# Optimization experiments

Hardware: AMD Instinct MI355X
Metric: run time of the kernel (lower is better)

The kernel has to match this reference:

```python
import jax, jax.numpy as jnp
import numpy as np
from jax import lax

NUM_SEGMENTS = 50
HIDDEN = 128
IN_CH = 64
LOGSIG_DIM = IN_CH + IN_CH * (IN_CH - 1) // 2 + IN_CH  # level1 + Levy area + startpoint


def setup_inputs() -> dict:
    key = jax.random.key(0)
    k0, k1, k2, k3, k4 = jax.random.split(key, 5)
    B, C, T, V = 16, IN_CH, 200, 25
    x = jax.random.normal(k0, (B, C, T, V), dtype=jnp.float32)
    s = 1.0 / np.sqrt(HIDDEN).astype(np.float32)
    W_ih = jax.random.uniform(k1, (4 * HIDDEN, LOGSIG_DIM), jnp.float32, -s, s)
    W_hh = jax.random.uniform(k2, (4 * HIDDEN, HIDDEN), jnp.float32, -s, s)
    b_ih = jax.random.uniform(k3, (4 * HIDDEN,), jnp.float32, -s, s)
    b_hh = jax.random.uniform(k4, (4 * HIDDEN,), jnp.float32, -s, s)
    return {"x": x, "W_ih": W_ih, "W_hh": W_hh, "b_ih": b_ih, "b_hh": b_hh}


def _segment_logsig(xn):
    # xn: (N, C, T). Split T into NUM_SEGMENTS chunks; level-2 log-signature per chunk.
    N, C, T = xn.shape
    L = T // NUM_SEGMENTS  # points per segment
    p = xn.transpose(0, 2, 1).reshape(N, NUM_SEGMENTS, L, C)  # path points
    start = p[:, :, 0]                                  # (N,S,C) segment startpoint
    inc = p[:, :, 1:] - p[:, :, :-1]                    # (N,S,L-1,C) increments
    dev = p[:, :, :-1] - start[:, :, None]              # (N,S,L-1,C) p_t - p_0
    # Level-2 iterated integrals (cross terms): S2_ij = sum_t dev_t,i * inc_t,j
    S2 = jnp.einsum('nsti,nstj->nsij', dev, inc)        # (N,S,C,C)
    A = 0.5 * (S2 - S2.transpose(0, 1, 3, 2))           # Levy area (antisymmetric part)
    iu, ju = jnp.triu_indices(C, k=1)
    levy = A[:, :, iu, ju]                              # (N,S,C(C-1)/2)
    lvl1 = p[:, :, -1] - start                          # (N,S,C) level-1 term
    return jnp.concatenate([lvl1, levy, start], axis=-1)  # (N,S,LOGSIG_DIM)


def _lstm(seq, W_ih, W_hh, b_ih, b_hh):
    # seq: (N, S, F). Single-layer unidirectional LSTM, torch gate order (i,f,g,o).
    N = seq.shape[0]
    x_proj = jnp.einsum('nsf,gf->nsg', seq, W_ih) + b_ih + b_hh  # (N,S,4H)

    def step(carry, xt):
        h, c = carry
        gates = xt + h @ W_hh.T
        i, f, g, o = jnp.split(gates, 4, axis=-1)
        c = jax.nn.sigmoid(f) * c + jax.nn.sigmoid(i) * jnp.tanh(g)
        h = jax.nn.sigmoid(o) * jnp.tanh(c)
        return (h, c), h

    h0 = jnp.zeros((N, HIDDEN), seq.dtype)
    c0 = jnp.zeros((N, HIDDEN), seq.dtype)
    _, hs = lax.scan(step, (h0, c0), x_proj.transpose(1, 0, 2))
    return hs.transpose(1, 0, 2)  # (N,S,H)


def reference(x, W_ih, W_hh, b_ih, b_hh):
    B, C, T, V = x.shape
    xn = x.transpose(0, 3, 1, 2).reshape(B * V, C, T)
    ls = _segment_logsig(xn)                      # (B*V, S, LOGSIG_DIM)
    h = _lstm(ls, W_ih, W_hh, b_ih, b_hh)          # (B*V, S, H)
    out = h.reshape(B, V, NUM_SEGMENTS, HIDDEN).transpose(0, 3, 2, 1)
    return out  # (B, H, S, V)
```

## Files before the change

kernel.cpp:

```cpp
#include <hip/hip_runtime.h>
#include <stdint.h>

#define NSEG 50
#define HID 128
#define KDIM 2144
#define KD2 2240
#define KD2B 4480
#define NROW 20000
#define NROW_PAD 20096
#define GATES 512
#define NSEQ 400
#define NGRP 528

typedef __attribute__((ext_vector_type(8))) _Float16 f16x8;
typedef __attribute__((ext_vector_type(4))) _Float16 f16x4;
typedef __attribute__((ext_vector_type(4))) float f32x4;
typedef __attribute__((ext_vector_type(4))) uint32_t u32x4;

#define GLB_SPACE __attribute__((address_space(1)))
#define LDS_SPACE __attribute__((address_space(3)))

__device__ __forceinline__ void g2lds16(const void* g, void* l) {
    __builtin_amdgcn_global_load_lds((const GLB_SPACE uint32_t*)g,
                                     (LDS_SPACE uint32_t*)l, 16, 0, 0);
}

__device__ __forceinline__ int goff528(int i) {
    int n = 63 - i;
    int q = n >> 2, t = n & 3;
    return NGRP - (q + 1) * (2 * q + t);
}
__device__ __forceinline__ int ifromg(int g) {
    int i = 63 - (int)sqrtf(8.0f * (float)(NGRP - g));
    if (i < 0) i = 0;
    if (i > 62) i = 62;
    while (i > 0 && goff528(i) > g) i--;
    while (goff528(i + 1) <= g) i++;
    return i;
}

#define UVP(c) ((((c) & 3) << 4) | ((c) >> 2))

__global__ __launch_bounds__(512) void feat_kernel(const float* __restrict__ x,
                                                   const float* __restrict__ Wih,
                                                   const float* __restrict__ Whh,
                                                   const float* __restrict__ bih,
                                                   const float* __restrict__ bhh,
                                                   _Float16* __restrict__ feat,
                                                   _Float16* __restrict__ wh,
                                                   _Float16* __restrict__ whh16,
                                                   float* __restrict__ bias) {
    int bid = blockIdx.x;
    int tid = threadIdx.x;

    __shared__ float pbuf[64 * 101];
    __shared__ __align__(16) float4 uv4[25 * 64];

    if (bid >= 800) {
        int* kmap = (int*)pbuf;
        for (int k = tid; k < KD2; k += 512) {
            int orig;
            if (k < 64) {
                orig = k;
            } else if (k < 64 + 4 * NGRP) {
                int g = (k - 64) >> 2, p = (k - 64) & 3;
                int i = ifromg(g);
                int j = i + 1 + 4 * (g - goff528(i)) + p;
                orig = (j < 64) ? (64 + 63 * i - (i * (i - 1)) / 2 + (j - i - 1)) : -1;
            } else {
                orig = 2080 + (k - (64 + 4 * NGRP));
            }
            kmap[k] = orig;
        }
        __syncthreads();
        const int nwih = 512 * KD2;
        const int nwhh = 512 * HID;
        const int total = nwih + nwhh + 512;
        for (int idx = (bid - 800) * 512 + tid; idx < total; idx += 64 * 512) {
            if (idx < nwih) {
                int row = idx / KD2;
                int k = idx - row * KD2;
                int orig = kmap[k];
                wh[idx] = (orig >= 0) ? (_Float16)Wih[row * KDIM + orig] : (_Float16)0.0f;
            } else if (idx < nwih + nwhh) {
                int q = idx - nwih;
                whh16[q] = (_Float16)Whh[q];
            } else {
                int g = idx - nwih - nwhh;
                bias[g] = bih[g] + bhh[g];
            }
        }
        return;
    }

    int b = bid / NSEG;
    int s = bid - b * NSEG;

    for (int i = tid; i < 6400; i += 512) {
        int c = i / 100;
        int r = i - c * 100;
        pbuf[c * 101 + r] = x[(((size_t)b * 64 + c) * 200 + 4 * s) * 25 + r];
    }
    __syncthreads();

    for (int i = tid; i < 1600; i += 512) {
        int v = i >> 6;
        int c = i & 63;
        float p0 = pbuf[c * 101 + v];
        float p1 = pbuf[c * 101 + 25 + v];
        float p2 = pbuf[c * 101 + 50 + v];
        float p3 = pbuf[c * 101 + 75 + v];
        uv4[v * 64 + UVP(c)] = make_float4(p1 - p0, p2 - p0, p2 - p1, p3 - p2);
        size_t m = ((size_t)(b * 25 + v)) * NSEG + s;
        feat[m * KD2 + c] = (_Float16)(p3 - p0);
        feat[m * KD2 + (64 + 4 * NGRP) + c] = (_Float16)p0;
    }
    __syncthreads();

    for (int g = tid; g < NGRP; g += 512) {
        int i = ifromg(g);
        int t = g - goff528(i);
        int j0 = i + 1 + 4 * t;
        int k0 = 64 + 4 * g;
        float msk[4];
        int jc[4];
#pragma unroll
        for (int p = 0; p < 4; p++) {
            int j = j0 + p;
            msk[p] = (j < 64) ? 0.5f : 0.0f;
            jc[p] = (j < 64) ? UVP(j) : UVP(63);
        }
        int ip = UVP(i);
        for (int v = 0; v < 25; v++) {
            const float4* rowv = &uv4[v * 64];
            float4 a = rowv[ip];
            f16x4 o;
#pragma unroll
            for (int p = 0; p < 4; p++) {
                float4 bb = rowv[jc[p]];
                float val = msk[p] * (a.x * bb.z - bb.x * a.z + a.y * bb.w - bb.y * a.w);
                o[p] = (_Float16)val;
            }
            size_t m = ((size_t)(b * 25 + v)) * NSEG + s;
            *(f16x4*)(feat + m * KD2 + k0) = o;
        }
    }
}

__global__ __launch_bounds__(256, 4) void gemm_kernel(const _Float16* __restrict__ feat,
                                                      const _Float16* __restrict__ wh,
                                                      const float* __restrict__ bias,
                                                      _Float16* __restrict__ xproj2) {
    int bid = blockIdx.x;
    int x = bid & 7;
    int t = bid >> 3;
    int nb = t & 3;
    int mt = (t >> 2) * 8 + x;
    if (mt >= 157) return;
    int m0 = mt * 128;
    int n0 = nb * 128;
    int tid = threadIdx.x;
    int wave = tid >> 6;
    int lane = tid & 63;
    int quad = lane >> 4;
    int l15 = lane & 15;
    int wm = (wave >> 1) * 64;
    int wn = (wave & 1) * 64;

    int r8 = lane >> 3;
    int gcol = ((lane & 7) * 16) ^ (r8 * 16);

    __shared__ __align__(16) _Float16 smem[16896];
    char* As = (char*)smem;
    char* Bs = (char*)smem + 128 * 128;

    const f32x4 z4 = {0.f, 0.f, 0.f, 0.f};
    f32x4 acc[4][4];
    for (int i = 0; i < 4; i++)
        for (int j = 0; j < 4; j++) acc[i][j] = z4;

    const char* featB = (const char*)feat;
    const char* whB = (const char*)wh;

    for (int kt = 0; kt < 35; kt++) {
        size_t kb = (size_t)kt * 128;
        __syncthreads();
        for (int it = 0; it < 4; it++) {
            int rb = it * 32 + wave * 8;
            g2lds16(featB + (size_t)(m0 + rb + r8) * KD2B + kb + gcol, As + rb * 128);
            g2lds16(whB + (size_t)(n0 + rb + r8) * KD2B + kb + gcol, Bs + rb * 128);
        }
        __syncthreads();

        for (int ks = 0; ks < 2; ks++) {
            int off = ((ks * 64) | (quad * 16)) ^ ((l15 & 7) * 16);
            f16x8 af[4], bf[4];
            for (int tt = 0; tt < 4; tt++)
                af[tt] = *(const f16x8*)(As + (wm + tt * 16 + l15) * 128 + off);
            for (int tt = 0; tt < 4; tt++)
                bf[tt] = *(const f16x8*)(Bs + (wn + tt * 16 + l15) * 128 + off);
            for (int mtl = 0; mtl < 4; mtl++)
                for (int ntl = 0; ntl < 4; ntl++)
                    acc[mtl][ntl] = __builtin_amdgcn_mfma_f32_16x16x32_f16(af[mtl], bf[ntl], acc[mtl][ntl], 0, 0, 0);
        }
    }

    __syncthreads();
    for (int ntl = 0; ntl < 4; ntl++) {
        int nl = wn + ntl * 16 + l15;
        float bv = bias[n0 + nl];
        for (int mtl = 0; mtl < 4; mtl++)
            for (int r = 0; r < 4; r++) {
                int ml = wm + mtl * 16 + quad * 4 + r;
                smem[ml * 132 + nl] = (_Float16)(acc[mtl][ntl][r] + bv);
            }
    }
    __syncthreads();
    {
        int row = tid >> 1;
        int half = tid & 1;
        int m = m0 + row;
        if (m < NROW) {
            unsigned q = (unsigned)m / 50u;
            unsigned s = (unsigned)m - q * 50u;
            const char* src = (const char*)smem + row * 264 + half * 128;
            char* dst = (char*)xproj2 + ((size_t)s * NSEQ + q) * 1024 + (size_t)n0 * 2 + half * 128;
            for (int i = 0; i < 8; i++)
                *(u32x4*)(dst + i * 16) = *(const u32x4*)(src + i * 16);
        }
    }
}

__global__ __launch_bounds__(512, 2) void lstm_kernel(const _Float16* __restrict__ xproj2,
                                                      const _Float16* __restrict__ whh,
                                                      _Float16* __restrict__ hseq) {
    int bid = blockIdx.x;
    int tid = threadIdx.x;
    int wave = tid >> 6;
    int lane = tid & 63;
    int quad = lane >> 4;
    int col = lane & 15;
    int hid = wave * 16 + col;

    __shared__ __align__(16) char xbuf[25 * 4 * 1040];
    __shared__ __align__(16) _Float16 hst[NSEG * 4 * HID];
    __shared__ __align__(16) _Float16 hbuf[2][4 * 144];

    f16x8 bfrag[4][4];
    for (int g = 0; g < 4; g++) {
        int n = g * 128 + hid;
        for (int kq = 0; kq < 4; kq++)
            bfrag[g][kq] = *(const f16x8*)(whh + (size_t)n * HID + kq * 32 + quad * 8);
    }
    for (int i = tid; i < 2 * 4 * 144; i += 512) ((_Float16*)hbuf)[i] = (_Float16)0.0f;
    float cst = 0.0f;

    const char* xsrc = (const char*)xproj2;
    for (int r = wave; r < 100; r += 8)
        g2lds16(xsrc + ((size_t)((r >> 2) * NSEQ + bid * 4 + (r & 3))) * 1024 + lane * 16,
                xbuf + r * 1040);
    __syncthreads();

    const f32x4 z4 = {0.f, 0.f, 0.f, 0.f};
    for (int half = 0; half < 2; half++) {
        for (int ss = 0; ss < 25; ss++) {
            int s = half * 25 + ss;
            int cur = s & 1;
            int nxt = cur ^ 1;

            f16x8 afrag[4];
            for (int kq = 0; kq < 4; kq++)
                afrag[kq] = *(const f16x8*)(&hbuf[cur][(col & 3) * 144 + kq * 32 + quad * 8]);

            float xp[4];
            for (int g = 0; g < 4; g++)
                xp[g] = (float)(*(const _Float16*)(xbuf + (ss * 4 + quad) * 1040 +
                               (g * 128 + hid) * 2));

            f32x4 acc[4];
            for (int g = 0; g < 4; g++) {
                acc[g] = z4;
                for (int kq = 0; kq < 4; kq++)
                    acc[g] = __builtin_amdgcn_mfma_f32_16x16x32_f16(afrag[kq], bfrag[g][kq], acc[g], 0, 0, 0);
            }

            float gv[4];
            for (int g = 0; g < 4; g++) {
                float lo = (quad & 1) ? acc[g][1] : acc[g][0];
                float hi = (quad & 1) ? acc[g][3] : acc[g][2];
                gv[g] = (quad & 2) ? hi : lo;
            }

            float ip = gv[0] + xp[0];
            float fp = gv[1] + xp[1];
            float gp = gv[2] + xp[2];
            float op = gv[3] + xp[3];
            float si = __fdividef(1.0f, 1.0f + __expf(-ip));
            float sf = __fdividef(1.0f, 1.0f + __expf(-fp));
            float so = __fdividef(1.0f, 1.0f + __expf(-op));
            float eg = __expf(-2.0f * gp);
            float tg = __fdividef(1.0f - eg, 1.0f + eg);
            cst = sf * cst + si * tg;
            float ec = __expf(-2.0f * cst);
            float tc = __fdividef(1.0f - ec, 1.0f + ec);
            float hv = so * tc;
            _Float16 hv16 = (_Float16)hv;
            hbuf[nxt][quad * 144 + hid] = hv16;
            hst[(s * 4 + quad) * 128 + hid] = hv16;
            __syncthreads();
        }
        if (half == 0) {
            for (int r = wave; r < 100; r += 8)
                g2lds16(xsrc + ((size_t)((25 + (r >> 2)) * NSEQ + bid * 4 + (r & 3))) * 1024 + lane * 16,
                        xbuf + r * 1040);
            __syncthreads();
        }
    }

    const u32x4* src = (const u32x4*)hst;
    for (int i = tid; i < 3200; i += 512) {
        int s = i >> 6;
        int rem = i & 63;
        int seq = rem >> 4;
        int seg = rem & 15;
        u32x4 v = src[i];
        *(u32x4*)((char*)hseq + ((size_t)(s * NSEQ + bid * 4 + seq)) * 256 + seg * 16) = v;
    }
}

__global__ __launch_bounds__(256) void tr_kernel(const _Float16* __restrict__ hseq,
                                                 float* __restrict__ out) {
    int bid = blockIdx.x;
    int b = bid / NSEG;
    int s = bid - b * NSEG;
    int tid = threadIdx.x;

    __shared__ _Float16 buf[25 * 130];

    const uint32_t* src32 = (const uint32_t*)(hseq + ((size_t)s * NSEQ + b * 25) * HID);
    uint32_t* buf32 = (uint32_t*)buf;
    for (int i = tid; i < 1600; i += 256) {
        int v = i >> 6;
        int d = i & 63;
        buf32[v * 65 + d] = src32[i];
    }
    __syncthreads();
    for (int i = tid; i < 3200; i += 256) {
        int hid = i / 25;
        int v = i - hid * 25;
        out[(((size_t)b * 128 + hid) * NSEG + s) * 25 + v] = (float)buf[v * 130 + hid];
    }
}

extern "C" void kernel_launch(void* const* d_in, const int* in_sizes, int n_in,
                              void* d_out, int out_size, void* d_ws, size_t ws_size,
                              hipStream_t stream) {
    const float* x = (const float*)d_in[0];
    const float* Wih = (const float*)d_in[1];
    const float* Whh = (const float*)d_in[2];
    const float* bih = (const float*)d_in[3];
    const float* bhh = (const float*)d_in[4];
    float* out = (float*)d_out;

    char* ws = (char*)d_ws;
    size_t off = 0;
    _Float16* feat = (_Float16*)(ws + off);   off += (size_t)NROW_PAD * KD2 * 2;
    _Float16* xproj2 = (_Float16*)(ws + off); off += (size_t)NSEG * NSEQ * GATES * 2;
    _Float16* hseq = (_Float16*)(ws + off);   off += (size_t)NSEG * NSEQ * HID * 2;
    _Float16* wh = (_Float16*)(ws + off);     off += (size_t)512 * KD2 * 2;
    _Float16* whh16 = (_Float16*)(ws + off);  off += (size_t)512 * HID * 2;
    float* bias = (float*)(ws + off);         off += 512 * 4;

    hipLaunchKernelGGL(feat_kernel, dim3(864), dim3(512), 0, stream,
                       x, Wih, Whh, bih, bhh, feat, wh, whh16, bias);
    hipLaunchKernelGGL(gemm_kernel, dim3(640), dim3(256), 0, stream, feat, wh, bias, xproj2);
    hipLaunchKernelGGL(lstm_kernel, dim3(100), dim3(512), 0, stream, xproj2, whh16, hseq);
    hipLaunchKernelGGL(tr_kernel, dim3(16 * NSEG), dim3(256), 0, stream, hseq, out);
}
```

Baseline: 212.7 us.

## Double-buffer GEMM LDS tiles and split logsig Levy work across v-blocks

The GEMM kernel now uses two LDS buffers so the async global-to-LDS load of the next K tile is issued before computing on the current one, which cuts one barrier per iteration and overlaps load with MFMA. Launch bounds drop to 2 blocks per CU to fit the doubled shared memory. The logsig kernel's Levy-area loop is split over four groups of v values so more threads in each block do useful work. The trade-off is lower occupancy in the GEMM.

```diff
diff --git a/kernel.cpp b/kernel.cpp
--- a/kernel.cpp
+++ b/kernel.cpp
@@ -117,7 +117,9 @@
     }
     __syncthreads();
 
-    for (int g = tid; g < NGRP; g += 512) {
+    for (int idx = tid; idx < 4 * NGRP; idx += 512) {
+        int vb = idx / NGRP;
+        int g = idx - vb * NGRP;
         int i = ifromg(g);
         int t = g - goff528(i);
         int j0 = i + 1 + 4 * t;
@@ -131,7 +133,10 @@
             jc[p] = (j < 64) ? UVP(j) : UVP(63);
         }
         int ip = UVP(i);
-        for (int v = 0; v < 25; v++) {
+        int v0 = (vb == 0) ? 0 : 6 * vb + 1;
+        int vn = (vb == 0) ? 7 : 6;
+        for (int vv = 0; vv < vn; vv++) {
+            int v = v0 + vv;
             const float4* rowv = &uv4[v * 64];
             float4 a = rowv[ip];
             f16x4 o;
@@ -147,7 +152,7 @@
     }
 }
 
-__global__ __launch_bounds__(256, 4) void gemm_kernel(const _Float16* __restrict__ feat,
+__global__ __launch_bounds__(256, 2) void gemm_kernel(const _Float16* __restrict__ feat,
                                                       const _Float16* __restrict__ wh,
                                                       const float* __restrict__ bias,
                                                       _Float16* __restrict__ xproj2) {
@@ -170,9 +175,7 @@
     int r8 = lane >> 3;
     int gcol = ((lane & 7) * 16) ^ (r8 * 16);
 
-    __shared__ __align__(16) _Float16 smem[16896];
-    char* As = (char*)smem;
-    char* Bs = (char*)smem + 128 * 128;
+    __shared__ __align__(16) _Float16 smem[2][16384];
 
     const f32x4 z4 = {0.f, 0.f, 0.f, 0.f};
     f32x4 acc[4][4];
@@ -182,37 +185,66 @@
     const char* featB = (const char*)feat;
     const char* whB = (const char*)wh;
 
-    for (int kt = 0; kt < 35; kt++) {
-        size_t kb = (size_t)kt * 128;
-        __syncthreads();
+    const char* aSrc[4];
+    const char* bSrc[4];
+#pragma unroll
+    for (int it = 0; it < 4; it++) {
+        int rb = it * 32 + wave * 8;
+        aSrc[it] = featB + (size_t)(m0 + rb + r8) * KD2B + gcol;
+        bSrc[it] = whB + (size_t)(n0 + rb + r8) * KD2B + gcol;
+    }
+
+    {
+        char* As = (char*)smem[0];
+        char* Bs = (char*)smem[0] + 16384;
+#pragma unroll
         for (int it = 0; it < 4; it++) {
             int rb = it * 32 + wave * 8;
-            g2lds16(featB + (size_t)(m0 + rb + r8) * KD2B + kb + gcol, As + rb * 128);
-            g2lds16(whB + (size_t)(n0 + rb + r8) * KD2B + kb + gcol, Bs + rb * 128);
+            g2lds16(aSrc[it], As + rb * 128);
+            g2lds16(bSrc[it], Bs + rb * 128);
+        }
+    }
+    __syncthreads();
+
+    for (int kt = 0; kt < 35; kt++) {
+        int cur = kt & 1;
+        if (kt + 1 < 35) {
+            size_t kb = (size_t)(kt + 1) * 128;
+            char* As = (char*)smem[cur ^ 1];
+            char* Bs = (char*)smem[cur ^ 1] + 16384;
+#pragma unroll
+            for (int it = 0; it < 4; it++) {
+                int rb = it * 32 + wave * 8;
+                g2lds16(aSrc[it] + kb, As + rb * 128);
+                g2lds16(bSrc[it] + kb, Bs + rb * 128);
+            }
+        }
+        {
+            const char* As = (const char*)smem[cur];
+            const char* Bs = (const char*)smem[cur] + 16384;
+            for (int ks = 0; ks < 2; ks++) {
+                int off = ((ks * 64) | (quad * 16)) ^ ((l15 & 7) * 16);
+                f16x8 af[4], bf[4];
+                for (int tt = 0; tt < 4; tt++)
+                    af[tt] = *(const f16x8*)(As + (wm + tt * 16 + l15) * 128 + off);
+                for (int tt = 0; tt < 4; tt++)
+                    bf[tt] = *(const f16x8*)(Bs + (wn + tt * 16 + l15) * 128 + off);
+                for (int mtl = 0; mtl < 4; mtl++)
+                    for (int ntl = 0; ntl < 4; ntl++)
+                        acc[mtl][ntl] = __builtin_amdgcn_mfma_f32_16x16x32_f16(af[mtl], bf[ntl], acc[mtl][ntl], 0, 0, 0);
+            }
         }
         __syncthreads();
-
-        for (int ks = 0; ks < 2; ks++) {
-            int off = ((ks * 64) | (quad * 16)) ^ ((l15 & 7) * 16);
-            f16x8 af[4], bf[4];
-            for (int tt = 0; tt < 4; tt++)
-                af[tt] = *(const f16x8*)(As + (wm + tt * 16 + l15) * 128 + off);
-            for (int tt = 0; tt < 4; tt++)
-                bf[tt] = *(const f16x8*)(Bs + (wn + tt * 16 + l15) * 128 + off);
-            for (int mtl = 0; mtl < 4; mtl++)
-                for (int ntl = 0; ntl < 4; ntl++)
-                    acc[mtl][ntl] = __builtin_amdgcn_mfma_f32_16x16x32_f16(af[mtl], bf[ntl], acc[mtl][ntl], 0, 0, 0);
-        }
-    }
-
-    __syncthreads();
+    }
+
+    _Float16* ep = (_Float16*)smem;
     for (int ntl = 0; ntl < 4; ntl++) {
         int nl = wn + ntl * 16 + l15;
         float bv = bias[n0 + nl];
         for (int mtl = 0; mtl < 4; mtl++)
             for (int r = 0; r < 4; r++) {
                 int ml = wm + mtl * 16 + quad * 4 + r;
-                smem[ml * 132 + nl] = (_Float16)(acc[mtl][ntl][r] + bv);
+                ep[ml * 132 + nl] = (_Float16)(acc[mtl][ntl][r] + bv);
             }
     }
     __syncthreads();
@@ -223,7 +255,7 @@
         if (m < NROW) {
             unsigned q = (unsigned)m / 50u;
             unsigned s = (unsigned)m - q * 50u;
-            const char* src = (const char*)smem + row * 264 + half * 128;
+            const char* src = (const char*)ep + row * 264 + half * 128;
             char* dst = (char*)xproj2 + ((size_t)s * NSEQ + q) * 1024 + (size_t)n0 * 2 + half * 128;
             for (int i = 0; i < 8; i++)
                 *(u32x4*)(dst + i * 16) = *(const u32x4*)(src + i * 16);
```

New measurement: 226.4 us. 1.06x slower.
